# Performance work log

Hardware: AMD Instinct MI355X
Metric: run time of the kernel (lower is better)

## Reference

```python
import jax, jax.numpy as jnp
import numpy as np

SORB = 64      # spin orbitals (sequence length)
NELE = 32      # electrons
H = 512        # num_hiddens
B = 4096       # batch
ALPHA = NELE // 2                      # = beta = 16 (spin-up / spin-down electrons)
MIN_I = min(SORB - 2 * ALPHA, 2 * ALPHA)  # = 32; symmetry mask active for i >= MIN_I
EPS = 1e-12


def setup_inputs() -> dict:
    key = jax.random.key(0)
    ks = jax.random.split(key, 10)
    s_in = 1.0 / np.sqrt(2.0)
    s_h = 1.0 / np.sqrt(H)
    return {
        "x": jax.random.randint(ks[0], (B, SORB), 0, 2, dtype=jnp.int32),  # occupancies {0,1}
        "W_ih0": jax.random.normal(ks[1], (3 * H, 2), jnp.float32) * s_in,   # GRU layer0 input weights (r,z,n)
        "W_hh0": jax.random.normal(ks[2], (3 * H, H), jnp.float32) * s_h,
        "W_ih1": jax.random.normal(ks[3], (3 * H, H), jnp.float32) * s_h,    # GRU layer1
        "W_hh1": jax.random.normal(ks[4], (3 * H, H), jnp.float32) * s_h,
        "W_amp": jax.random.normal(ks[5], (2, H), jnp.float32) * s_h,
        "b_amp": jax.random.normal(ks[6], (2,), jnp.float32) * 0.01,
        "W_phase": jax.random.normal(ks[7], (2, H), jnp.float32) * s_h,
        "b_phase": jax.random.normal(ks[8], (2,), jnp.float32) * 0.01,
    }


def _gru_cell(x_in, h, Wih, Whh):
    # PyTorch GRU (bias=False), gate order r, z, n
    gi = x_in @ Wih.T          # (B, 3H)
    gh = h @ Whh.T             # (B, 3H)
    r = jax.nn.sigmoid(gi[:, :H] + gh[:, :H])
    z = jax.nn.sigmoid(gi[:, H:2 * H] + gh[:, H:2 * H])
    n = jnp.tanh(gi[:, 2 * H:] + r * gh[:, 2 * H:])
    return (1.0 - z) * n + z * h


def reference(x, W_ih0, W_hh0, W_ih1, W_hh1, W_amp, b_amp, W_phase, b_phase):
    dt = W_ih0.dtype
    bits = x.astype(jnp.int32)           # (B, SORB) occupancies
    nb = bits.shape[0]

    def step(carry, inp):
        h0, h1, x0, amp, phase, nup, ndn = carry
        i, b_i = inp                      # site index, occupancy bits (B,)
        h0n = _gru_cell(x0, h0, W_ih0, W_hh0)
        h1n = _gru_cell(h0n, h1, W_ih1, W_hh1)
        y = h1n                           # (B, H)
        # amplitude: sqrt(softmax(linear))
        y_amp = jnp.sqrt(jax.nn.softmax(y @ W_amp.T + b_amp, axis=1))   # (B, 2)
        # phase: pi * softsign(linear)
        ph = y @ W_phase.T + b_phase
        y_ph = jnp.pi * ph / (1.0 + jnp.abs(ph))
        # particle-number symmetry mask (alpha == beta spin sectors)
        is_even = (i % 2) == 0            # even sites: spin-up, odd: spin-down
        cnt = jnp.where(is_even, nup, ndn)
        lower = (ALPHA - SORB // 2 + i // 2).astype(dt)
        occ_ok = (cnt < ALPHA).astype(dt)
        unocc_ok = (cnt > lower).astype(dt)
        mask = jnp.stack([unocc_ok, occ_ok], axis=1)
        masked = y_amp * mask
        masked = masked / jnp.sqrt(jnp.sum(masked * masked, axis=1, keepdims=True) + EPS)
        y_amp = jnp.where(i >= MIN_I, masked, y_amp)
        # accumulate conditional amplitude / phase at the sampled occupancy
        sel_a = jnp.take_along_axis(y_amp, b_i[:, None], axis=1)[:, 0]
        sel_p = jnp.take_along_axis(y_ph, b_i[:, None], axis=1)[:, 0]
        amp = amp * sel_a
        phase = phase + sel_p
        bf = b_i.astype(dt)
        nup = nup + jnp.where(is_even, bf, 0.0)
        ndn = ndn + jnp.where(is_even, 0.0, bf)
        x0n = jax.nn.one_hot(b_i, 2, dtype=dt)  # next-step GRU input
        return (h0n, h1n, x0n, amp, phase, nup, ndn), None

    init = (
        jnp.zeros((nb, H), dt), jnp.zeros((nb, H), dt), jnp.zeros((nb, 2), dt),
        jnp.ones((nb,), dt), jnp.zeros((nb,), dt), jnp.zeros((nb,), dt), jnp.zeros((nb,), dt),
    )
    xs = (jnp.arange(SORB), bits.T)       # scan over sites
    (_, _, _, amp, phase, _, _), _ = jax.lax.scan(step, init, xs)
    # complex wavefunction psi = amp * exp(1j*phase); returned as real pair (amp, phase)
    return jnp.stack([amp, phase], axis=-1)
```

## Files before the change

### kernel.cpp

```cpp
#include <hip/hip_runtime.h>
#include <hip/hip_bf16.h>

#define SORB  64
#define HID   512
#define BATCH 4096
#define N3H   1536
#define KD    512
#define BK    64
#define PI_F  3.14159265358979f

typedef _Float16 half8 __attribute__((ext_vector_type(8)));
typedef float    floatx4 __attribute__((ext_vector_type(4)));

__device__ __forceinline__ void gload16(const void* g, void* l) {
    __builtin_amdgcn_global_load_lds(
        (const __attribute__((address_space(1))) void*)g,
        (__attribute__((address_space(3))) void*)l, 16, 0, 0);
}

__device__ __forceinline__ float sigmoidf_(float x) { return 1.f / (1.f + __expf(-x)); }
__device__ __forceinline__ float tanhf_(float x) {
    x = fminf(fmaxf(x, -15.f), 15.f);
    const float e2 = __expf(2.f * x);
    return (e2 - 1.f) / (e2 + 1.f);
}

__global__ __launch_bounds__(256) void convw_kernel(
    const float* __restrict__ w0, const float* __restrict__ w1, const float* __restrict__ w2,
    _Float16* __restrict__ o0, _Float16* __restrict__ o1, _Float16* __restrict__ o2)
{
    const int i = blockIdx.x * 256 + threadIdx.x;
    if (i < N3H * KD) {
        o0[i] = (_Float16)w0[i];
        o1[i] = (_Float16)w1[i];
        o2[i] = (_Float16)w2[i];
    }
}

__global__ __launch_bounds__(256) void init_kernel(
    float* __restrict__ amp, float* __restrict__ phase,
    int* __restrict__ nup, int* __restrict__ ndn)
{
    const int i = blockIdx.x * 256 + threadIdx.x;
    if (i < BATCH) { amp[i] = 1.f; phase[i] = 0.f; nup[i] = 0; ndn[i] = 0; }
}


__global__ __launch_bounds__(256) void step1_kernel(
    const _Float16* __restrict__ h0h_c, const _Float16* __restrict__ h1h_c,
    const _Float16* __restrict__ wh0,   const _Float16* __restrict__ wh1,
    const float* __restrict__ Wih0, const int* __restrict__ bits,
    float* __restrict__ h0f, _Float16* __restrict__ h0h_n,
    _Float16* __restrict__ gB, int step)
{
    const int z = blockIdx.z;
    const _Float16* A = z ? h1h_c : h0h_c;
    const _Float16* W = z ? wh1 : wh0;
    const int j0 = blockIdx.x * 64;
    const int m0 = blockIdx.y * 64;

    __shared__ __align__(16) _Float16 As[64 * BK];
    __shared__ __align__(16) _Float16 Bs[192 * BK];

    const int tid  = threadIdx.x;
    const int lane = tid & 63;
    const int wid  = tid >> 6;
    const int wm   = wid >> 1, wj = wid & 1;

    floatx4 acc[2][2][3];
    const floatx4 z4 = {0.f, 0.f, 0.f, 0.f};
#pragma unroll
    for (int a = 0; a < 2; ++a)
#pragma unroll
        for (int b = 0; b < 2; ++b)
#pragma unroll
            for (int g = 0; g < 3; ++g) acc[a][b][g] = z4;

    const _Float16* a_srcp[2];
#pragma unroll
    for (int k2 = 0; k2 < 2; ++k2) {
        const int p = tid + k2 * 256, row = p >> 3, c = (p & 7) ^ (row & 7);
        a_srcp[k2] = A + (size_t)(m0 + row) * KD + c * 8;
    }
    const _Float16* b_srcp[6];
#pragma unroll
    for (int k2 = 0; k2 < 6; ++k2) {
        const int p = tid + k2 * 256, row = p >> 3, c = (p & 7) ^ (row & 7);
        const int grow = (row >> 6) * HID + j0 + (row & 63);
        b_srcp[k2] = W + (size_t)grow * KD + c * 8;
    }
    _Float16* a_dst[2];
#pragma unroll
    for (int k2 = 0; k2 < 2; ++k2) a_dst[k2] = As + (size_t)(k2 * 256 + wid * 64) * 8;
    _Float16* b_dst[6];
#pragma unroll
    for (int k2 = 0; k2 < 6; ++k2) b_dst[k2] = Bs + (size_t)(k2 * 256 + wid * 64) * 8;

    const int ku = lane >> 4;
    int aoff[2][2], boff[2][3][2];
#pragma unroll
    for (int mf = 0; mf < 2; ++mf) {
        const int r = wm * 32 + mf * 16 + (lane & 15);
#pragma unroll
        for (int kk = 0; kk < 2; ++kk)
            aoff[mf][kk] = r * BK + (((kk * 4 + ku) ^ (r & 7)) * 8);
    }
#pragma unroll
    for (int jf = 0; jf < 2; ++jf)
#pragma unroll
        for (int g = 0; g < 3; ++g) {
            const int r = g * 64 + wj * 32 + jf * 16 + (lane & 15);
#pragma unroll
            for (int kk = 0; kk < 2; ++kk)
                boff[jf][g][kk] = r * BK + (((kk * 4 + ku) ^ (r & 7)) * 8);
        }

    for (int kt = 0; kt < 8; ++kt) {
        const int k0 = kt * BK;
#pragma unroll
        for (int k2 = 0; k2 < 2; ++k2) gload16(a_srcp[k2] + k0, a_dst[k2]);
#pragma unroll
        for (int k2 = 0; k2 < 6; ++k2) gload16(b_srcp[k2] + k0, b_dst[k2]);
        __syncthreads();
#pragma unroll
        for (int kk = 0; kk < 2; ++kk) {
            half8 af[2], bf[2][3];
#pragma unroll
            for (int mf = 0; mf < 2; ++mf) af[mf] = *(const half8*)(As + aoff[mf][kk]);
#pragma unroll
            for (int jf = 0; jf < 2; ++jf)
#pragma unroll
                for (int g = 0; g < 3; ++g) bf[jf][g] = *(const half8*)(Bs + boff[jf][g][kk]);
#pragma unroll
            for (int mf = 0; mf < 2; ++mf)
#pragma unroll
                for (int jf = 0; jf < 2; ++jf)
#pragma unroll
                    for (int g = 0; g < 3; ++g)
                        acc[mf][jf][g] = __builtin_amdgcn_mfma_f32_16x16x32_f16(af[mf], bf[jf][g], acc[mf][jf][g], 0, 0, 0);
        }
        __syncthreads();
    }

    if (z == 0) {
#pragma unroll
        for (int mf = 0; mf < 2; ++mf)
#pragma unroll
            for (int jf = 0; jf < 2; ++jf) {
                const floatx4 gr = acc[mf][jf][0];
                const floatx4 gz = acc[mf][jf][1];
                const floatx4 gn = acc[mf][jf][2];
#pragma unroll
                for (int reg = 0; reg < 4; ++reg) {
                    const int m = m0 + wm * 32 + mf * 16 + (lane >> 4) * 4 + reg;
                    const int j = j0 + wj * 32 + jf * 16 + (lane & 15);
                    float gir = 0.f, giz = 0.f, gin = 0.f;
                    if (step > 0) {
                        const int t = bits[m * SORB + step - 1];
                        gir = Wih0[j * 2 + t];
                        giz = Wih0[(HID + j) * 2 + t];
                        gin = Wih0[(2 * HID + j) * 2 + t];
                    }
                    const float r  = sigmoidf_(gir + gr[reg]);
                    const float zz = sigmoidf_(giz + gz[reg]);
                    const float n  = tanhf_(gin + r * gn[reg]);
                    const size_t idx = (size_t)m * HID + j;
                    const float h  = h0f[idx];
                    const float hn = (1.f - zz) * n + zz * h;
                    h0f[idx]   = hn;
                    h0h_n[idx] = (_Float16)hn;
                }
            }
    } else {
#pragma unroll
        for (int mf = 0; mf < 2; ++mf)
#pragma unroll
            for (int jf = 0; jf < 2; ++jf)
#pragma unroll
                for (int g = 0; g < 3; ++g)
#pragma unroll
                    for (int reg = 0; reg < 4; ++reg) {
                        const int m = m0 + wm * 32 + mf * 16 + (lane >> 4) * 4 + reg;
                        const int j = j0 + wj * 32 + jf * 16 + (lane & 15);
                        gB[(size_t)m * N3H + g * HID + j] = (_Float16)acc[mf][jf][g][reg];
                    }
    }
}

__global__ __launch_bounds__(256) void step2_kernel(
    const _Float16* __restrict__ h0h_n, const _Float16* __restrict__ wi1,
    const _Float16* __restrict__ gB,
    float* __restrict__ h1f, _Float16* __restrict__ h1h_n)
{
    const int j0 = blockIdx.x * 64;
    const int m0 = blockIdx.y * 64;

    __shared__ __align__(16) _Float16 As[64 * BK];
    __shared__ __align__(16) _Float16 Bs[192 * BK];

    const int tid  = threadIdx.x;
    const int lane = tid & 63;
    const int wid  = tid >> 6;
    const int wm   = wid >> 1, wj = wid & 1;

    floatx4 acc[2][2][3];
    const floatx4 z4 = {0.f, 0.f, 0.f, 0.f};
#pragma unroll
    for (int a = 0; a < 2; ++a)
#pragma unroll
        for (int b = 0; b < 2; ++b)
#pragma unroll
            for (int g = 0; g < 3; ++g) acc[a][b][g] = z4;

    const _Float16* a_srcp[2];
#pragma unroll
    for (int k2 = 0; k2 < 2; ++k2) {
        const int p = tid + k2 * 256, row = p >> 3, c = (p & 7) ^ (row & 7);
        a_srcp[k2] = h0h_n + (size_t)(m0 + row) * KD + c * 8;
    }
    const _Float16* b_srcp[6];
#pragma unroll
    for (int k2 = 0; k2 < 6; ++k2) {
        const int p = tid + k2 * 256, row = p >> 3, c = (p & 7) ^ (row & 7);
        const int grow = (row >> 6) * HID + j0 + (row & 63);
        b_srcp[k2] = wi1 + (size_t)grow * KD + c * 8;
    }
    _Float16* a_dst[2];
#pragma unroll
    for (int k2 = 0; k2 < 2; ++k2) a_dst[k2] = As + (size_t)(k2 * 256 + wid * 64) * 8;
    _Float16* b_dst[6];
#pragma unroll
    for (int k2 = 0; k2 < 6; ++k2) b_dst[k2] = Bs + (size_t)(k2 * 256 + wid * 64) * 8;

    const int ku = lane >> 4;
    int aoff[2][2], boff[2][3][2];
#pragma unroll
    for (int mf = 0; mf < 2; ++mf) {
        const int r = wm * 32 + mf * 16 + (lane & 15);
#pragma unroll
        for (int kk = 0; kk < 2; ++kk)
            aoff[mf][kk] = r * BK + (((kk * 4 + ku) ^ (r & 7)) * 8);
    }
#pragma unroll
    for (int jf = 0; jf < 2; ++jf)
#pragma unroll
        for (int g = 0; g < 3; ++g) {
            const int r = g * 64 + wj * 32 + jf * 16 + (lane & 15);
#pragma unroll
            for (int kk = 0; kk < 2; ++kk)
                boff[jf][g][kk] = r * BK + (((kk * 4 + ku) ^ (r & 7)) * 8);
        }

    for (int kt = 0; kt < 8; ++kt) {
        const int k0 = kt * BK;
#pragma unroll
        for (int k2 = 0; k2 < 2; ++k2) gload16(a_srcp[k2] + k0, a_dst[k2]);
#pragma unroll
        for (int k2 = 0; k2 < 6; ++k2) gload16(b_srcp[k2] + k0, b_dst[k2]);
        __syncthreads();
#pragma unroll
        for (int kk = 0; kk < 2; ++kk) {
            half8 af[2], bf[2][3];
#pragma unroll
            for (int mf = 0; mf < 2; ++mf) af[mf] = *(const half8*)(As + aoff[mf][kk]);
#pragma unroll
            for (int jf = 0; jf < 2; ++jf)
#pragma unroll
                for (int g = 0; g < 3; ++g) bf[jf][g] = *(const half8*)(Bs + boff[jf][g][kk]);
#pragma unroll
            for (int mf = 0; mf < 2; ++mf)
#pragma unroll
                for (int jf = 0; jf < 2; ++jf)
#pragma unroll
                    for (int g = 0; g < 3; ++g)
                        acc[mf][jf][g] = __builtin_amdgcn_mfma_f32_16x16x32_f16(af[mf], bf[jf][g], acc[mf][jf][g], 0, 0, 0);
        }
        __syncthreads();
    }

#pragma unroll
    for (int mf = 0; mf < 2; ++mf)
#pragma unroll
        for (int jf = 0; jf < 2; ++jf) {
            const floatx4 gr = acc[mf][jf][0];
            const floatx4 gz = acc[mf][jf][1];
            const floatx4 gn = acc[mf][jf][2];
#pragma unroll
            for (int reg = 0; reg < 4; ++reg) {
                const int m = m0 + wm * 32 + mf * 16 + (lane >> 4) * 4 + reg;
                const int j = j0 + wj * 32 + jf * 16 + (lane & 15);
                const size_t gbase = (size_t)m * N3H;
                const float ghr = (float)gB[gbase + j];
                const float ghz = (float)gB[gbase + HID + j];
                const float ghn = (float)gB[gbase + 2 * HID + j];
                const float r  = sigmoidf_(gr[reg] + ghr);
                const float zz = sigmoidf_(gz[reg] + ghz);
                const float n  = tanhf_(gn[reg] + r * ghn);
                const size_t idx = (size_t)m * HID + j;
                const float h  = h1f[idx];
                const float hn = (1.f - zz) * n + zz * h;
                h1f[idx]   = hn;
                h1h_n[idx] = (_Float16)hn;
            }
        }
}

__global__ __launch_bounds__(256) void head_kernel(
    const _Float16* __restrict__ h1h_n,
    const float* __restrict__ Wamp, const float* __restrict__ bamp,
    const float* __restrict__ Wph,  const float* __restrict__ bph,
    const int* __restrict__ bits,
    float* __restrict__ amp, float* __restrict__ phase,
    int* __restrict__ nup, int* __restrict__ ndn,
    float* __restrict__ out, int step)
{
    const int lane = threadIdx.x & 63;
    const int m    = blockIdx.x * 4 + (threadIdx.x >> 6);
    const half8 hv = *(const half8*)(h1h_n + (size_t)m * HID + lane * 8);
    float d0 = 0.f, d1 = 0.f, d2 = 0.f, d3 = 0.f;
#pragma unroll
    for (int e = 0; e < 8; ++e) {
        const int j = lane * 8 + e;
        const float hn = (float)hv[e];
        d0 += hn * Wamp[j];       d1 += hn * Wamp[HID + j];
        d2 += hn * Wph[j];        d3 += hn * Wph[HID + j];
    }
#pragma unroll
    for (int off = 1; off < 64; off <<= 1) {
        d0 += __shfl_xor(d0, off); d1 += __shfl_xor(d1, off);
        d2 += __shfl_xor(d2, off); d3 += __shfl_xor(d3, off);
    }
    if (lane == 0) {
        const float a0 = d0 + bamp[0];
        const float a1 = d1 + bamp[1];
        const float mx = fmaxf(a0, a1);
        const float e0 = __expf(a0 - mx), e1 = __expf(a1 - mx);
        const float inv = 1.f / (e0 + e1);
        float ya0 = sqrtf(e0 * inv), ya1 = sqrtf(e1 * inv);
        const float p0 = d2 + bph[0];
        const float p1 = d3 + bph[1];
        const float yp0 = PI_F * p0 / (1.f + fabsf(p0));
        const float yp1 = PI_F * p1 / (1.f + fabsf(p1));
        const int even = ((step & 1) == 0);
        const int cnt = even ? nup[m] : ndn[m];
        if (step >= 32) {
            const int lower = (step >> 1) - 16;
            const float m0v = (cnt > lower) ? ya0 : 0.f;
            const float m1v = (cnt < 16) ? ya1 : 0.f;
            const float nrm = sqrtf(m0v * m0v + m1v * m1v + 1e-12f);
            ya0 = m0v / nrm; ya1 = m1v / nrm;
        }
        const int bi = bits[m * SORB + step];
        const float na = amp[m] * (bi ? ya1 : ya0);
        const float np = phase[m] + (bi ? yp1 : yp0);
        amp[m] = na; phase[m] = np;
        if (bi) { if (even) nup[m] = cnt + 1; else ndn[m] = cnt + 1; }
        if (step == SORB - 1) {
            out[m * 2 + 0] = na;
            out[m * 2 + 1] = np;
        }
    }
}

extern "C" void kernel_launch(void* const* d_in, const int* in_sizes, int n_in,
                              void* d_out, int out_size, void* d_ws, size_t ws_size,
                              hipStream_t stream) {
    const int*   bits = (const int*)d_in[0];
    const float* Wih0 = (const float*)d_in[1];
    const float* Whh0 = (const float*)d_in[2];
    const float* Wih1 = (const float*)d_in[3];
    const float* Whh1 = (const float*)d_in[4];
    const float* Wamp = (const float*)d_in[5];
    const float* bamp = (const float*)d_in[6];
    const float* Wph  = (const float*)d_in[7];
    const float* bph  = (const float*)d_in[8];
    float* out = (float*)d_out;

    char* ws = (char*)d_ws;
    size_t off = 0;
    auto alloc = [&](size_t bytes) {
        void* p = ws + off;
        off = (off + bytes + 255) & ~(size_t)255;
        return p;
    };
    _Float16* wh0 = (_Float16*)alloc((size_t)N3H * KD * 2);
    _Float16* wi1 = (_Float16*)alloc((size_t)N3H * KD * 2);
    _Float16* wh1 = (_Float16*)alloc((size_t)N3H * KD * 2);
    float*    h0f = (float*)alloc((size_t)BATCH * HID * 4);
    float*    h1f = (float*)alloc((size_t)BATCH * HID * 4);
    _Float16* h0hA = (_Float16*)alloc((size_t)BATCH * HID * 2);
    _Float16* h0hB = (_Float16*)alloc((size_t)BATCH * HID * 2);
    _Float16* h1hA = (_Float16*)alloc((size_t)BATCH * HID * 2);
    _Float16* h1hB = (_Float16*)alloc((size_t)BATCH * HID * 2);
    _Float16* gB  = (_Float16*)alloc((size_t)BATCH * N3H * 2);
    float*    amp   = (float*)alloc((size_t)BATCH * 4);
    float*    phase = (float*)alloc((size_t)BATCH * 4);
    int*      nup   = (int*)alloc((size_t)BATCH * 4);
    int*      ndn   = (int*)alloc((size_t)BATCH * 4);

    _Float16* h0h[2] = {h0hA, h0hB};
    _Float16* h1h[2] = {h1hA, h1hB};

    hipMemsetAsync(h0f, 0, (size_t)BATCH * HID * 4, stream);
    hipMemsetAsync(h1f, 0, (size_t)BATCH * HID * 4, stream);
    hipMemsetAsync(h0hA, 0, (size_t)BATCH * HID * 2, stream);
    hipMemsetAsync(h1hA, 0, (size_t)BATCH * HID * 2, stream);
    convw_kernel<<<(N3H * KD + 255) / 256, 256, 0, stream>>>(Whh0, Wih1, Whh1, wh0, wi1, wh1);
    init_kernel<<<BATCH / 256, 256, 0, stream>>>(amp, phase, nup, ndn);

    for (int s = 0; s < SORB; ++s) {
        const int cur = s & 1, nxt = cur ^ 1;
        step1_kernel<<<dim3(8, 64, 2), 256, 0, stream>>>(
            h0h[cur], h1h[cur], wh0, wh1, Wih0, bits, h0f, h0h[nxt], gB, s);
        step2_kernel<<<dim3(8, 64, 1), 256, 0, stream>>>(
            h0h[nxt], wi1, gB, h1f, h1h[nxt]);
        head_kernel<<<BATCH / 4, 256, 0, stream>>>(
            h1h[nxt], Wamp, bamp, Wph, bph, bits, amp, phase, nup, ndn, out, s);
    }
}
```

Baseline: 3.307 ms.

## Fold head computation into next step's layer-1 GEMM blocks and remap grid

Removes the per-step head kernel launch. The head for step s-1 now runs in the z=1 blocks of the next step1 launch, reading the previous h1 buffer, and only the final step's head runs as a standalone launch after the loop. The grid is flattened to 1024 blocks and interleaved so that z=0 and z=1 tiles alternate in groups of four. This saves 63 launches and their drain gaps, at the cost of extra tail work in the z=1 blocks, which could unbalance them against the z=0 blocks.

Measured after the change: 3.623 ms. 1.1x slower.

```diff
diff --git a/kernel.cpp b/kernel.cpp
--- a/kernel.cpp
+++ b/kernel.cpp
@@ -45,278 +45,16 @@
     if (i < BATCH) { amp[i] = 1.f; phase[i] = 0.f; nup[i] = 0; ndn[i] = 0; }
 }
 
-
-__global__ __launch_bounds__(256) void step1_kernel(
-    const _Float16* __restrict__ h0h_c, const _Float16* __restrict__ h1h_c,
-    const _Float16* __restrict__ wh0,   const _Float16* __restrict__ wh1,
-    const float* __restrict__ Wih0, const int* __restrict__ bits,
-    float* __restrict__ h0f, _Float16* __restrict__ h0h_n,
-    _Float16* __restrict__ gB, int step)
-{
-    const int z = blockIdx.z;
-    const _Float16* A = z ? h1h_c : h0h_c;
-    const _Float16* W = z ? wh1 : wh0;
-    const int j0 = blockIdx.x * 64;
-    const int m0 = blockIdx.y * 64;
-
-    __shared__ __align__(16) _Float16 As[64 * BK];
-    __shared__ __align__(16) _Float16 Bs[192 * BK];
-
-    const int tid  = threadIdx.x;
-    const int lane = tid & 63;
-    const int wid  = tid >> 6;
-    const int wm   = wid >> 1, wj = wid & 1;
-
-    floatx4 acc[2][2][3];
-    const floatx4 z4 = {0.f, 0.f, 0.f, 0.f};
-#pragma unroll
-    for (int a = 0; a < 2; ++a)
-#pragma unroll
-        for (int b = 0; b < 2; ++b)
-#pragma unroll
-            for (int g = 0; g < 3; ++g) acc[a][b][g] = z4;
-
-    const _Float16* a_srcp[2];
-#pragma unroll
-    for (int k2 = 0; k2 < 2; ++k2) {
-        const int p = tid + k2 * 256, row = p >> 3, c = (p & 7) ^ (row & 7);
-        a_srcp[k2] = A + (size_t)(m0 + row) * KD + c * 8;
-    }
-    const _Float16* b_srcp[6];
-#pragma unroll
-    for (int k2 = 0; k2 < 6; ++k2) {
-        const int p = tid + k2 * 256, row = p >> 3, c = (p & 7) ^ (row & 7);
-        const int grow = (row >> 6) * HID + j0 + (row & 63);
-        b_srcp[k2] = W + (size_t)grow * KD + c * 8;
-    }
-    _Float16* a_dst[2];
-#pragma unroll
-    for (int k2 = 0; k2 < 2; ++k2) a_dst[k2] = As + (size_t)(k2 * 256 + wid * 64) * 8;
-    _Float16* b_dst[6];
-#pragma unroll
-    for (int k2 = 0; k2 < 6; ++k2) b_dst[k2] = Bs + (size_t)(k2 * 256 + wid * 64) * 8;
-
-    const int ku = lane >> 4;
-    int aoff[2][2], boff[2][3][2];
-#pragma unroll
-    for (int mf = 0; mf < 2; ++mf) {
-        const int r = wm * 32 + mf * 16 + (lane & 15);
-#pragma unroll
-        for (int kk = 0; kk < 2; ++kk)
-            aoff[mf][kk] = r * BK + (((kk * 4 + ku) ^ (r & 7)) * 8);
-    }
-#pragma unroll
-    for (int jf = 0; jf < 2; ++jf)
-#pragma unroll
-        for (int g = 0; g < 3; ++g) {
-            const int r = g * 64 + wj * 32 + jf * 16 + (lane & 15);
-#pragma unroll
-            for (int kk = 0; kk < 2; ++kk)
-                boff[jf][g][kk] = r * BK + (((kk * 4 + ku) ^ (r & 7)) * 8);
-        }
-
-    for (int kt = 0; kt < 8; ++kt) {
-        const int k0 = kt * BK;
-#pragma unroll
-        for (int k2 = 0; k2 < 2; ++k2) gload16(a_srcp[k2] + k0, a_dst[k2]);
-#pragma unroll
-        for (int k2 = 0; k2 < 6; ++k2) gload16(b_srcp[k2] + k0, b_dst[k2]);
-        __syncthreads();
-#pragma unroll
-        for (int kk = 0; kk < 2; ++kk) {
-            half8 af[2], bf[2][3];
-#pragma unroll
-            for (int mf = 0; mf < 2; ++mf) af[mf] = *(const half8*)(As + aoff[mf][kk]);
-#pragma unroll
-            for (int jf = 0; jf < 2; ++jf)
-#pragma unroll
-                for (int g = 0; g < 3; ++g) bf[jf][g] = *(const half8*)(Bs + boff[jf][g][kk]);
-#pragma unroll
-            for (int mf = 0; mf < 2; ++mf)
-#pragma unroll
-                for (int jf = 0; jf < 2; ++jf)
-#pragma unroll
-                    for (int g = 0; g < 3; ++g)
-                        acc[mf][jf][g] = __builtin_amdgcn_mfma_f32_16x16x32_f16(af[mf], bf[jf][g], acc[mf][jf][g], 0, 0, 0);
-        }
-        __syncthreads();
-    }
-
-    if (z == 0) {
-#pragma unroll
-        for (int mf = 0; mf < 2; ++mf)
-#pragma unroll
-            for (int jf = 0; jf < 2; ++jf) {
-                const floatx4 gr = acc[mf][jf][0];
-                const floatx4 gz = acc[mf][jf][1];
-                const floatx4 gn = acc[mf][jf][2];
-#pragma unroll
-                for (int reg = 0; reg < 4; ++reg) {
-                    const int m = m0 + wm * 32 + mf * 16 + (lane >> 4) * 4 + reg;
-                    const int j = j0 + wj * 32 + jf * 16 + (lane & 15);
-                    float gir = 0.f, giz = 0.f, gin = 0.f;
-                    if (step > 0) {
-                        const int t = bits[m * SORB + step - 1];
-                        gir = Wih0[j * 2 + t];
-                        giz = Wih0[(HID + j) * 2 + t];
-                        gin = Wih0[(2 * HID + j) * 2 + t];
-                    }
-                    const float r  = sigmoidf_(gir + gr[reg]);
-                    const float zz = sigmoidf_(giz + gz[reg]);
-                    const float n  = tanhf_(gin + r * gn[reg]);
-                    const size_t idx = (size_t)m * HID + j;
-                    const float h  = h0f[idx];
-                    const float hn = (1.f - zz) * n + zz * h;
-                    h0f[idx]   = hn;
-                    h0h_n[idx] = (_Float16)hn;
-                }
-            }
-    } else {
-#pragma unroll
-        for (int mf = 0; mf < 2; ++mf)
-#pragma unroll
-            for (int jf = 0; jf < 2; ++jf)
-#pragma unroll
-                for (int g = 0; g < 3; ++g)
-#pragma unroll
-                    for (int reg = 0; reg < 4; ++reg) {
-                        const int m = m0 + wm * 32 + mf * 16 + (lane >> 4) * 4 + reg;
-                        const int j = j0 + wj * 32 + jf * 16 + (lane & 15);
-                        gB[(size_t)m * N3H + g * HID + j] = (_Float16)acc[mf][jf][g][reg];
-                    }
-    }
-}
-
-__global__ __launch_bounds__(256) void step2_kernel(
-    const _Float16* __restrict__ h0h_n, const _Float16* __restrict__ wi1,
-    const _Float16* __restrict__ gB,
-    float* __restrict__ h1f, _Float16* __restrict__ h1h_n)
-{
-    const int j0 = blockIdx.x * 64;
-    const int m0 = blockIdx.y * 64;
-
-    __shared__ __align__(16) _Float16 As[64 * BK];
-    __shared__ __align__(16) _Float16 Bs[192 * BK];
-
-    const int tid  = threadIdx.x;
-    const int lane = tid & 63;
-    const int wid  = tid >> 6;
-    const int wm   = wid >> 1, wj = wid & 1;
-
-    floatx4 acc[2][2][3];
-    const floatx4 z4 = {0.f, 0.f, 0.f, 0.f};
-#pragma unroll
-    for (int a = 0; a < 2; ++a)
-#pragma unroll
-        for (int b = 0; b < 2; ++b)
-#pragma unroll
-            for (int g = 0; g < 3; ++g) acc[a][b][g] = z4;
-
-    const _Float16* a_srcp[2];
-#pragma unroll
-    for (int k2 = 0; k2 < 2; ++k2) {
-        const int p = tid + k2 * 256, row = p >> 3, c = (p & 7) ^ (row & 7);
-        a_srcp[k2] = h0h_n + (size_t)(m0 + row) * KD + c * 8;
-    }
-    const _Float16* b_srcp[6];
-#pragma unroll
-    for (int k2 = 0; k2 < 6; ++k2) {
-        const int p = tid + k2 * 256, row = p >> 3, c = (p & 7) ^ (row & 7);
-        const int grow = (row >> 6) * HID + j0 + (row & 63);
-        b_srcp[k2] = wi1 + (size_t)grow * KD + c * 8;
-    }
-    _Float16* a_dst[2];
-#pragma unroll
-    for (int k2 = 0; k2 < 2; ++k2) a_dst[k2] = As + (size_t)(k2 * 256 + wid * 64) * 8;
-    _Float16* b_dst[6];
-#pragma unroll
-    for (int k2 = 0; k2 < 6; ++k2) b_dst[k2] = Bs + (size_t)(k2 * 256 + wid * 64) * 8;
-
-    const int ku = lane >> 4;
-    int aoff[2][2], boff[2][3][2];
-#pragma unroll
-    for (int mf = 0; mf < 2; ++mf) {
-        const int r = wm * 32 + mf * 16 + (lane & 15);
-#pragma unroll
-        for (int kk = 0; kk < 2; ++kk)
-            aoff[mf][kk] = r * BK + (((kk * 4 + ku) ^ (r & 7)) * 8);
-    }
-#pragma unroll
-    for (int jf = 0; jf < 2; ++jf)
-#pragma unroll
-        for (int g = 0; g < 3; ++g) {
-            const int r = g * 64 + wj * 32 + jf * 16 + (lane & 15);
-#pragma unroll
-            for (int kk = 0; kk < 2; ++kk)
-                boff[jf][g][kk] = r * BK + (((kk * 4 + ku) ^ (r & 7)) * 8);
-        }
-
-    for (int kt = 0; kt < 8; ++kt) {
-        const int k0 = kt * BK;
-#pragma unroll
-        for (int k2 = 0; k2 < 2; ++k2) gload16(a_srcp[k2] + k0, a_dst[k2]);
-#pragma unroll
-        for (int k2 = 0; k2 < 6; ++k2) gload16(b_srcp[k2] + k0, b_dst[k2]);
-        __syncthreads();
-#pragma unroll
-        for (int kk = 0; kk < 2; ++kk) {
-            half8 af[2], bf[2][3];
-#pragma unroll
-            for (int mf = 0; mf < 2; ++mf) af[mf] = *(const half8*)(As + aoff[mf][kk]);
-#pragma unroll
-            for (int jf = 0; jf < 2; ++jf)
-#pragma unroll
-                for (int g = 0; g < 3; ++g) bf[jf][g] = *(const half8*)(Bs + boff[jf][g][kk]);
-#pragma unroll
-            for (int mf = 0; mf < 2; ++mf)
-#pragma unroll
-                for (int jf = 0; jf < 2; ++jf)
-#pragma unroll
-                    for (int g = 0; g < 3; ++g)
-                        acc[mf][jf][g] = __builtin_amdgcn_mfma_f32_16x16x32_f16(af[mf], bf[jf][g], acc[mf][jf][g], 0, 0, 0);
-        }
-        __syncthreads();
-    }
-
-#pragma unroll
-    for (int mf = 0; mf < 2; ++mf)
-#pragma unroll
-        for (int jf = 0; jf < 2; ++jf) {
-            const floatx4 gr = acc[mf][jf][0];
-            const floatx4 gz = acc[mf][jf][1];
-            const floatx4 gn = acc[mf][jf][2];
-#pragma unroll
-            for (int reg = 0; reg < 4; ++reg) {
-                const int m = m0 + wm * 32 + mf * 16 + (lane >> 4) * 4 + reg;
-                const int j = j0 + wj * 32 + jf * 16 + (lane & 15);
-                const size_t gbase = (size_t)m * N3H;
-                const float ghr = (float)gB[gbase + j];
-                const float ghz = (float)gB[gbase + HID + j];
-                const float ghn = (float)gB[gbase + 2 * HID + j];
-                const float r  = sigmoidf_(gr[reg] + ghr);
-                const float zz = sigmoidf_(gz[reg] + ghz);
-                const float n  = tanhf_(gn[reg] + r * ghn);
-                const size_t idx = (size_t)m * HID + j;
-                const float h  = h1f[idx];
-                const float hn = (1.f - zz) * n + zz * h;
-                h1f[idx]   = hn;
-                h1h_n[idx] = (_Float16)hn;
-            }
-        }
-}
-
-__global__ __launch_bounds__(256) void head_kernel(
-    const _Float16* __restrict__ h1h_n,
+__device__ __forceinline__ void head_row(
+    const _Float16* __restrict__ h1, int m,
     const float* __restrict__ Wamp, const float* __restrict__ bamp,
     const float* __restrict__ Wph,  const float* __restrict__ bph,
     const int* __restrict__ bits,
     float* __restrict__ amp, float* __restrict__ phase,
     int* __restrict__ nup, int* __restrict__ ndn,
-    float* __restrict__ out, int step)
-{
-    const int lane = threadIdx.x & 63;
-    const int m    = blockIdx.x * 4 + (threadIdx.x >> 6);
-    const half8 hv = *(const half8*)(h1h_n + (size_t)m * HID + lane * 8);
+    float* __restrict__ out, int step, int lane)
+{
+    const half8 hv = *(const half8*)(h1 + (size_t)m * HID + lane * 8);
     float d0 = 0.f, d1 = 0.f, d2 = 0.f, d3 = 0.f;
 #pragma unroll
     for (int e = 0; e < 8; ++e) {
@@ -360,6 +98,297 @@
             out[m * 2 + 1] = np;
         }
     }
+}
+
+__global__ __launch_bounds__(256) void step1_kernel(
+    const _Float16* __restrict__ h0h_c, const _Float16* __restrict__ h1h_c,
+    const _Float16* __restrict__ wh0,   const _Float16* __restrict__ wh1,
+    const float* __restrict__ Wih0, const int* __restrict__ bits,
+    float* __restrict__ h0f, _Float16* __restrict__ h0h_n,
+    _Float16* __restrict__ gB, int step,
+    const float* __restrict__ Wamp, const float* __restrict__ bamp,
+    const float* __restrict__ Wph,  const float* __restrict__ bph,
+    float* __restrict__ amp, float* __restrict__ phase,
+    int* __restrict__ nup, int* __restrict__ ndn, float* __restrict__ out)
+{
+    const int id  = blockIdx.x;
+    const int r8  = id & 7;
+    const int z   = (r8 >= 4) ? 1 : 0;
+    const int t   = (id >> 3) * 4 + (r8 & 3);
+    const int j0  = (t & 7) * 64;
+    const int m0  = (t >> 3) * 64;
+
+    const _Float16* Aop = z ? h1h_c : h0h_c;
+    const _Float16* Wop = z ? wh1 : wh0;
+
+    __shared__ __align__(16) _Float16 As[64 * BK];
+    __shared__ __align__(16) _Float16 Bs[192 * BK];
+
+    const int tid  = threadIdx.x;
+    const int lane = tid & 63;
+    const int wid  = tid >> 6;
+    const int wm   = wid >> 1, wj = wid & 1;
+    const int ku   = lane >> 4;
+
+    floatx4 acc[2][2][3];
+    const floatx4 z4 = {0.f, 0.f, 0.f, 0.f};
+#pragma unroll
+    for (int a = 0; a < 2; ++a)
+#pragma unroll
+        for (int b = 0; b < 2; ++b)
+#pragma unroll
+            for (int g = 0; g < 3; ++g) acc[a][b][g] = z4;
+
+    const _Float16* a_srcp[2];
+#pragma unroll
+    for (int k2 = 0; k2 < 2; ++k2) {
+        const int p = tid + k2 * 256, row = p >> 3, c = (p & 7) ^ (row & 7);
+        a_srcp[k2] = Aop + (size_t)(m0 + row) * KD + c * 8;
+    }
+    const _Float16* b_srcp[6];
+#pragma unroll
+    for (int k2 = 0; k2 < 6; ++k2) {
+        const int p = tid + k2 * 256, row = p >> 3, c = (p & 7) ^ (row & 7);
+        const int grow = (row >> 6) * HID + j0 + (row & 63);
+        b_srcp[k2] = Wop + (size_t)grow * KD + c * 8;
+    }
+    _Float16* a_dst[2];
+#pragma unroll
+    for (int k2 = 0; k2 < 2; ++k2) a_dst[k2] = As + (size_t)(k2 * 256 + wid * 64) * 8;
+    _Float16* b_dst[6];
+#pragma unroll
+    for (int k2 = 0; k2 < 6; ++k2) b_dst[k2] = Bs + (size_t)(k2 * 256 + wid * 64) * 8;
+
+    int aoff[2][2], boff[2][3][2];
+#pragma unroll
+    for (int mf = 0; mf < 2; ++mf) {
+        const int r = wm * 32 + mf * 16 + (lane & 15);
+#pragma unroll
+        for (int kk = 0; kk < 2; ++kk)
+            aoff[mf][kk] = r * BK + (((kk * 4 + ku) ^ (r & 7)) * 8);
+    }
+#pragma unroll
+    for (int jf = 0; jf < 2; ++jf)
+#pragma unroll
+        for (int g = 0; g < 3; ++g) {
+            const int r = g * 64 + wj * 32 + jf * 16 + (lane & 15);
+#pragma unroll
+            for (int kk = 0; kk < 2; ++kk)
+                boff[jf][g][kk] = r * BK + (((kk * 4 + ku) ^ (r & 7)) * 8);
+        }
+
+    for (int kt = 0; kt < 8; ++kt) {
+        const int k0 = kt * BK;
+#pragma unroll
+        for (int k2 = 0; k2 < 2; ++k2) gload16(a_srcp[k2] + k0, a_dst[k2]);
+#pragma unroll
+        for (int k2 = 0; k2 < 6; ++k2) gload16(b_srcp[k2] + k0, b_dst[k2]);
+        __syncthreads();
+#pragma unroll
+        for (int kk = 0; kk < 2; ++kk) {
+            half8 af[2], bf[2][3];
+#pragma unroll
+            for (int mf = 0; mf < 2; ++mf) af[mf] = *(const half8*)(As + aoff[mf][kk]);
+#pragma unroll
+            for (int jf = 0; jf < 2; ++jf)
+#pragma unroll
+                for (int g = 0; g < 3; ++g) bf[jf][g] = *(const half8*)(Bs + boff[jf][g][kk]);
+#pragma unroll
+            for (int mf = 0; mf < 2; ++mf)
+#pragma unroll
+                for (int jf = 0; jf < 2; ++jf)
+#pragma unroll
+                    for (int g = 0; g < 3; ++g)
+                        acc[mf][jf][g] = __builtin_amdgcn_mfma_f32_16x16x32_f16(
+                            af[mf], bf[jf][g], acc[mf][jf][g], 0, 0, 0);
+        }
+        __syncthreads();
+    }
+
+    if (z == 0) {
+#pragma unroll
+        for (int mf = 0; mf < 2; ++mf)
+#pragma unroll
+            for (int jf = 0; jf < 2; ++jf) {
+                const floatx4 gr = acc[mf][jf][0];
+                const floatx4 gz = acc[mf][jf][1];
+                const floatx4 gn = acc[mf][jf][2];
+#pragma unroll
+                for (int reg = 0; reg < 4; ++reg) {
+                    const int m = m0 + wm * 32 + mf * 16 + (lane >> 4) * 4 + reg;
+                    const int j = j0 + wj * 32 + jf * 16 + (lane & 15);
+                    float gir = 0.f, giz = 0.f, gin = 0.f;
+                    if (step > 0) {
+                        const int tb = bits[m * SORB + step - 1];
+                        gir = Wih0[j * 2 + tb];
+                        giz = Wih0[(HID + j) * 2 + tb];
+                        gin = Wih0[(2 * HID + j) * 2 + tb];
+                    }
+                    const float r  = sigmoidf_(gir + gr[reg]);
+                    const float zz = sigmoidf_(giz + gz[reg]);
+                    const float n  = tanhf_(gin + r * gn[reg]);
+                    const size_t idx = (size_t)m * HID + j;
+                    const float h  = h0f[idx];
+                    const float hn = (1.f - zz) * n + zz * h;
+                    h0f[idx]   = hn;
+                    h0h_n[idx] = (_Float16)hn;
+                }
+            }
+    } else {
+#pragma unroll
+        for (int mf = 0; mf < 2; ++mf)
+#pragma unroll
+            for (int jf = 0; jf < 2; ++jf)
+#pragma unroll
+                for (int g = 0; g < 3; ++g)
+#pragma unroll
+                    for (int reg = 0; reg < 4; ++reg) {
+                        const int m = m0 + wm * 32 + mf * 16 + (lane >> 4) * 4 + reg;
+                        const int j = j0 + wj * 32 + jf * 16 + (lane & 15);
+                        gB[(size_t)m * N3H + g * HID + j] = (_Float16)acc[mf][jf][g][reg];
+                    }
+        if (step > 0) {
+#pragma unroll
+            for (int rr = 0; rr < 2; ++rr) {
+                const int m = t * 8 + wid * 2 + rr;
+                head_row(h1h_c, m, Wamp, bamp, Wph, bph, bits,
+                         amp, phase, nup, ndn, out, step - 1, lane);
+            }
+        }
+    }
+}
+
+__global__ __launch_bounds__(256) void step2_kernel(
+    const _Float16* __restrict__ h0h_n, const _Float16* __restrict__ wi1,
+    const _Float16* __restrict__ gB,
+    float* __restrict__ h1f, _Float16* __restrict__ h1h_n)
+{
+    const int j0 = blockIdx.x * 64;
+    const int m0 = blockIdx.y * 64;
+
+    __shared__ __align__(16) _Float16 As[64 * BK];
+    __shared__ __align__(16) _Float16 Bs[192 * BK];
+
+    const int tid  = threadIdx.x;
+    const int lane = tid & 63;
+    const int wid  = tid >> 6;
+    const int wm   = wid >> 1, wj = wid & 1;
+    const int ku   = lane >> 4;
+
+    floatx4 acc[2][2][3];
+    const floatx4 z4 = {0.f, 0.f, 0.f, 0.f};
+#pragma unroll
+    for (int a = 0; a < 2; ++a)
+#pragma unroll
+        for (int b = 0; b < 2; ++b)
+#pragma unroll
+            for (int g = 0; g < 3; ++g) acc[a][b][g] = z4;
+
+    const _Float16* a_srcp[2];
+#pragma unroll
+    for (int k2 = 0; k2 < 2; ++k2) {
+        const int p = tid + k2 * 256, row = p >> 3, c = (p & 7) ^ (row & 7);
+        a_srcp[k2] = h0h_n + (size_t)(m0 + row) * KD + c * 8;
+    }
+    const _Float16* b_srcp[6];
+#pragma unroll
+    for (int k2 = 0; k2 < 6; ++k2) {
+        const int p = tid + k2 * 256, row = p >> 3, c = (p & 7) ^ (row & 7);
+        const int grow = (row >> 6) * HID + j0 + (row & 63);
+        b_srcp[k2] = wi1 + (size_t)grow * KD + c * 8;
+    }
+    _Float16* a_dst[2];
+#pragma unroll
+    for (int k2 = 0; k2 < 2; ++k2) a_dst[k2] = As + (size_t)(k2 * 256 + wid * 64) * 8;
+    _Float16* b_dst[6];
+#pragma unroll
+    for (int k2 = 0; k2 < 6; ++k2) b_dst[k2] = Bs + (size_t)(k2 * 256 + wid * 64) * 8;
+
+    int aoff[2][2], boff[2][3][2];
+#pragma unroll
+    for (int mf = 0; mf < 2; ++mf) {
+        const int r = wm * 32 + mf * 16 + (lane & 15);
+#pragma unroll
+        for (int kk = 0; kk < 2; ++kk)
+            aoff[mf][kk] = r * BK + (((kk * 4 + ku) ^ (r & 7)) * 8);
+    }
+#pragma unroll
+    for (int jf = 0; jf < 2; ++jf)
+#pragma unroll
+        for (int g = 0; g < 3; ++g) {
+            const int r = g * 64 + wj * 32 + jf * 16 + (lane & 15);
+#pragma unroll
+            for (int kk = 0; kk < 2; ++kk)
+                boff[jf][g][kk] = r * BK + (((kk * 4 + ku) ^ (r & 7)) * 8);
+        }
+
+    for (int kt = 0; kt < 8; ++kt) {
+        const int k0 = kt * BK;
+#pragma unroll
+        for (int k2 = 0; k2 < 2; ++k2) gload16(a_srcp[k2] + k0, a_dst[k2]);
+#pragma unroll
+        for (int k2 = 0; k2 < 6; ++k2) gload16(b_srcp[k2] + k0, b_dst[k2]);
+        __syncthreads();
+#pragma unroll
+        for (int kk = 0; kk < 2; ++kk) {
+            half8 af[2], bf[2][3];
+#pragma unroll
+            for (int mf = 0; mf < 2; ++mf) af[mf] = *(const half8*)(As + aoff[mf][kk]);
+#pragma unroll
+            for (int jf = 0; jf < 2; ++jf)
+#pragma unroll
+                for (int g = 0; g < 3; ++g) bf[jf][g] = *(const half8*)(Bs + boff[jf][g][kk]);
+#pragma unroll
+            for (int mf = 0; mf < 2; ++mf)
+#pragma unroll
+                for (int jf = 0; jf < 2; ++jf)
+#pragma unroll
+                    for (int g = 0; g < 3; ++g)
+                        acc[mf][jf][g] = __builtin_amdgcn_mfma_f32_16x16x32_f16(
+                            af[mf], bf[jf][g], acc[mf][jf][g], 0, 0, 0);
+        }
+        __syncthreads();
+    }
+
+#pragma unroll
+    for (int mf = 0; mf < 2; ++mf)
+#pragma unroll
+        for (int jf = 0; jf < 2; ++jf) {
+            const floatx4 gr = acc[mf][jf][0];
+            const floatx4 gz = acc[mf][jf][1];
+            const floatx4 gn = acc[mf][jf][2];
+#pragma unroll
+            for (int reg = 0; reg < 4; ++reg) {
+                const int m = m0 + wm * 32 + mf * 16 + (lane >> 4) * 4 + reg;
+                const int j = j0 + wj * 32 + jf * 16 + (lane & 15);
+                const size_t gbase = (size_t)m * N3H;
+                const float ghr = (float)gB[gbase + j];
+                const float ghz = (float)gB[gbase + HID + j];
+                const float ghn = (float)gB[gbase + 2 * HID + j];
+                const float r  = sigmoidf_(gr[reg] + ghr);
+                const float zz = sigmoidf_(gz[reg] + ghz);
+                const float n  = tanhf_(gn[reg] + r * ghn);
+                const size_t idx = (size_t)m * HID + j;
+                const float h  = h1f[idx];
+                const float hn = (1.f - zz) * n + zz * h;
+                h1f[idx]   = hn;
+                h1h_n[idx] = (_Float16)hn;
+            }
+        }
+}
+
+__global__ __launch_bounds__(256) void head_kernel(
+    const _Float16* __restrict__ h1h_n,
+    const float* __restrict__ Wamp, const float* __restrict__ bamp,
+    const float* __restrict__ Wph,  const float* __restrict__ bph,
+    const int* __restrict__ bits,
+    float* __restrict__ amp, float* __restrict__ phase,
+    int* __restrict__ nup, int* __restrict__ ndn,
+    float* __restrict__ out, int step)
+{
+    const int lane = threadIdx.x & 63;
+    const int m    = blockIdx.x * 4 + (threadIdx.x >> 6);
+    head_row(h1h_n, m, Wamp, bamp, Wph, bph, bits, amp, phase, nup, ndn, out, step, lane);
 }
 
 extern "C" void kernel_launch(void* const* d_in, const int* in_sizes, int n_in,
@@ -410,11 +439,12 @@
 
     for (int s = 0; s < SORB; ++s) {
         const int cur = s & 1, nxt = cur ^ 1;
-        step1_kernel<<<dim3(8, 64, 2), 256, 0, stream>>>(
-            h0h[cur], h1h[cur], wh0, wh1, Wih0, bits, h0f, h0h[nxt], gB, s);
-        step2_kernel<<<dim3(8, 64, 1), 256, 0, stream>>>(
+        step1_kernel<<<1024, 256, 0, stream>>>(
+            h0h[cur], h1h[cur], wh0, wh1, Wih0, bits, h0f, h0h[nxt], gB, s,
+            Wamp, bamp, Wph, bph, amp, phase, nup, ndn, out);
+        step2_kernel<<<dim3(8, 64), 256, 0, stream>>>(
             h0h[nxt], wi1, gB, h1f, h1h[nxt]);
-        head_kernel<<<BATCH / 4, 256, 0, stream>>>(
-            h1h[nxt], Wamp, bamp, Wph, bph, bits, amp, phase, nup, ndn, out, s);
-    }
-}
+    }
+    head_kernel<<<BATCH / 4, 256, 0, stream>>>(
+        h1h[0], Wamp, bamp, Wph, bph, bits, amp, phase, nup, ndn, out, SORB - 1);
+}
```
